# Kernel tuning notes

Measured on AMD Instinct MI355X. Metric: run time of the kernel, lower is better.

The kernel has to match this reference:

```python
import jax, jax.numpy as jnp
import numpy as np

MARGIN = 0.3
N, D, N_IDS = 8192, 128, 1024


def setup_inputs() -> dict:
    key = jax.random.key(0)
    k1, k2 = jax.random.split(key)
    inputs = jax.random.normal(k1, (N, D), dtype=jnp.float32)
    targets = jax.random.randint(k2, (N,), 0, N_IDS)
    return {"inputs": inputs, "targets": targets}


def reference(inputs, targets):
    # mask[i, j] = True iff sample j shares sample i's identity (includes j == i)
    mask = targets[:, None] == targets[None, :]               # [n, n] bool
    maskf = mask.astype(inputs.dtype)
    counts = maskf.sum(axis=1, keepdims=True)                 # [n, 1] (>= 1, self match)
    # center_i = mean of positives of sample i
    centers = (maskf @ inputs) / counts                       # [n, d]
    # squared distance from every center i to every sample j via gram expansion
    x2 = jnp.sum(inputs * inputs, axis=1)                     # [n]
    c2 = jnp.sum(centers * centers, axis=1)                   # [n]
    dist2 = c2[:, None] + x2[None, :] - 2.0 * (centers @ inputs.T)  # [n, n]
    # hard mining: farthest positive from center, closest negative to center
    dist_cp = jnp.where(mask, dist2, -jnp.inf).max(axis=1)    # [n]
    dist_cn = jnp.where(mask, jnp.inf, dist2).min(axis=1)     # [n]
    # MarginRankingLoss(y=1): mean(relu(-(dist_cn - dist_cp) + margin))
    loss = jnp.mean(jax.nn.relu(dist_cp - dist_cn + MARGIN))
    prec = jnp.mean((dist_cn > dist_cp).astype(jnp.float32))
    return loss, prec
```

## Files before the change

kernel.cpp:

```cpp
#include <hip/hip_runtime.h>
#include <math.h>

#define N_SAMPLES 8192
#define DIM 128
#define NCLS 1024
#define MARGIN_V 0.3f
#define DIST_GX (N_SAMPLES / 128)
#define DIST_GY (NCLS / 64)
#define NPART DIST_GX
#define MAXMEM 64
#define PIPE 16

using bf16x8 = __attribute__((ext_vector_type(8))) short;
using f32x16 = __attribute__((ext_vector_type(16))) float;
using short8 = __attribute__((ext_vector_type(8))) short;

__device__ __forceinline__ short bf16_rne(float x) {
  unsigned u = __float_as_uint(x);
  unsigned r = u + 0x7FFFu + ((u >> 16) & 1u);
  return (short)(r >> 16);
}

__device__ __forceinline__ size_t frag_idx(int row, int oct) {
  int tile = row >> 5, ks = oct >> 1, lane = ((oct & 1) << 5) | (row & 31);
  return (size_t)(tile * 8 + ks) * 64 + lane;
}

__global__ __launch_bounds__(256) void pack_kernel(
    const float* __restrict__ inputs, const int* __restrict__ targets,
    float* __restrict__ x2, float* __restrict__ c2, int* __restrict__ counts,
    short8* __restrict__ Apk, short8* __restrict__ Bpk, float* __restrict__ out) {
  int b = blockIdx.x;
  int tid = threadIdx.x;
  if (b == 0 && tid < 2) out[tid] = 0.f;
  if (b < N_SAMPLES / 16) {
    int row = b * 16 + (tid >> 4);
    int oct = tid & 15;
    const float4* p = (const float4*)(inputs + (size_t)row * DIM + oct * 8);
    float4 v0 = p[0], v1 = p[1];
    float v[8] = {v0.x, v0.y, v0.z, v0.w, v1.x, v1.y, v1.z, v1.w};
    float s = 0.f;
    #pragma unroll
    for (int i = 0; i < 8; i++) s += v[i] * v[i];
    #pragma unroll
    for (int m = 1; m < 16; m <<= 1) s += __shfl_xor(s, m);
    if (oct == 0) x2[row] = s;
    short8 hi;
    #pragma unroll
    for (int i = 0; i < 8; i++) hi[i] = bf16_rne(v[i]);
    Bpk[frag_idx(row, oct)] = hi;
  } else {
    __shared__ int mem[2][MAXMEM];
    __shared__ int mcnt[2];
    __shared__ float sctr[2][128];
    __shared__ float wsum[4];
    int c0 = (b - N_SAMPLES / 16) * 2;
    if (tid < 2) { mcnt[tid] = 0; mem[tid][0] = 0; }
    __syncthreads();
    int tg[N_SAMPLES / 256];
    #pragma unroll
    for (int i = 0; i < N_SAMPLES / 256; i++) tg[i] = targets[tid + 256 * i];
    #pragma unroll
    for (int i = 0; i < N_SAMPLES / 256; i++) {
      if (tg[i] == c0) {
        int p = atomicAdd(&mcnt[0], 1);
        if (p < MAXMEM) mem[0][p] = tid + 256 * i;
      } else if (tg[i] == c0 + 1) {
        int p = atomicAdd(&mcnt[1], 1);
        if (p < MAXMEM) mem[1][p] = tid + 256 * i;
      }
    }
    __syncthreads();
    int half = tid >> 7;
    int c = c0 + half;
    int d = tid & 127;
    int cnt = mcnt[half];
    int cl = (cnt < MAXMEM) ? cnt : MAXMEM;
    int n1 = (cl < PIPE) ? cl : PIPE;
    int idxs[PIPE];
    #pragma unroll
    for (int i = 0; i < PIPE; i++) idxs[i] = mem[half][(i < n1) ? i : 0];
    float vbuf[PIPE];
    #pragma unroll
    for (int i = 0; i < PIPE; i++) vbuf[i] = inputs[(size_t)idxs[i] * DIM + d];
    float acc = 0.f;
    #pragma unroll
    for (int i = 0; i < PIPE; i++) if (i < n1) acc += vbuf[i];
    for (int m = PIPE; m < cl; m++) acc += inputs[(size_t)mem[half][m] * DIM + d];
    float ctr = (cnt > 0) ? acc / (float)cnt : 0.f;
    sctr[half][d] = ctr;
    float vv = ctr * ctr;
    #pragma unroll
    for (int sh = 32; sh > 0; sh >>= 1) vv += __shfl_down(vv, sh);
    if ((tid & 63) == 0) wsum[tid >> 6] = vv;
    __syncthreads();
    if (d == 0) {
      c2[c] = wsum[half * 2] + wsum[half * 2 + 1];
      counts[c] = cnt;
    }
    if (d < 16) {
      int oct = d;
      short8 hi;
      #pragma unroll
      for (int i = 0; i < 8; i++) hi[i] = bf16_rne(sctr[half][oct * 8 + i]);
      Apk[frag_idx(c, oct)] = hi;
    }
  }
}

__global__ __launch_bounds__(256, 4) void dist_kernel(
    const short8* __restrict__ Apk, const short8* __restrict__ Bpk,
    const float* __restrict__ x2, const float* __restrict__ c2,
    const int* __restrict__ targets,
    float* __restrict__ dp_part, float* __restrict__ dn_part) {
  __shared__ float sc2[64];
  __shared__ float sx2[128];
  __shared__ int stgt[128];
  __shared__ float redp[2][2][32];
  __shared__ float redn[2][2][32];

  int tid = threadIdx.x;
  int jbase = blockIdx.x * 128;
  int cbase = blockIdx.y * 64;
  int wave = tid >> 6, lane = tid & 63;
  int wm = wave >> 1, wn = wave & 1;

  if (tid < 128) {
    sx2[tid] = x2[jbase + tid];
    stgt[tid] = targets[jbase + tid];
  }
  if (tid < 64) sc2[tid] = c2[cbase + tid];

  int mtg = (cbase >> 5) + wm;
  int ntg0 = (jbase >> 5) + wn * 2;

  f32x16 acc[2];
  acc[0] = (f32x16)(0.f);
  acc[1] = (f32x16)(0.f);

  #pragma unroll
  for (int ks = 0; ks < 8; ks++) {
    bf16x8 av = Apk[(size_t)(mtg * 8 + ks) * 64 + lane];
    bf16x8 b0 = Bpk[(size_t)((ntg0 + 0) * 8 + ks) * 64 + lane];
    bf16x8 b1 = Bpk[(size_t)((ntg0 + 1) * 8 + ks) * 64 + lane];
    acc[0] = __builtin_amdgcn_mfma_f32_32x32x16_bf16(av, b0, acc[0], 0, 0, 0);
    acc[1] = __builtin_amdgcn_mfma_f32_32x32x16_bf16(av, b1, acc[1], 0, 0, 0);
  }

  __syncthreads();

  int hf = lane >> 5;
  int col = lane & 31;
  #pragma unroll
  for (int r = 0; r < 16; r++) {
    int rowl = (r & 3) + 8 * (r >> 2) + 4 * hf;
    int c_loc = wm * 32 + rowl;
    int cg = cbase + c_loc;
    float c2v = sc2[c_loc];
    float pmax = -INFINITY, nmin = INFINITY;
    #pragma unroll
    for (int nt = 0; nt < 2; nt++) {
      int j_loc = wn * 64 + nt * 32 + col;
      float d2 = c2v + sx2[j_loc] - 2.f * acc[nt][r];
      if (stgt[j_loc] == cg) pmax = fmaxf(pmax, d2);
      else                   nmin = fminf(nmin, d2);
    }
    #pragma unroll
    for (int m = 1; m < 32; m <<= 1) {
      pmax = fmaxf(pmax, __shfl_xor(pmax, m));
      nmin = fminf(nmin, __shfl_xor(nmin, m));
    }
    if (col == 0) {
      redp[wn][wm][rowl] = pmax;
      redn[wn][wm][rowl] = nmin;
    }
  }
  __syncthreads();
  if (tid < 64) {
    int wmx = tid >> 5, idx = tid & 31;
    float dp = fmaxf(redp[0][wmx][idx], redp[1][wmx][idx]);
    float dn = fminf(redn[0][wmx][idx], redn[1][wmx][idx]);
    size_t slot = (size_t)blockIdx.x * NCLS + cbase + tid;
    dp_part[slot] = dp;
    dn_part[slot] = dn;
  }
}

__global__ __launch_bounds__(256) void finalize_kernel(
    const float* __restrict__ dp_part, const float* __restrict__ dn_part,
    const int* __restrict__ counts, float* __restrict__ out) {
  __shared__ float sdp[4][64];
  __shared__ float sdn[4][64];
  int g = blockIdx.x;
  int t = threadIdx.x;
  int cl = t & 63;
  int pg = t >> 6;
  int c = g * 64 + cl;
  float dp = -INFINITY, dn = INFINITY;
  #pragma unroll
  for (int p = pg * 16; p < pg * 16 + 16; p++) {
    dp = fmaxf(dp, dp_part[(size_t)p * NCLS + c]);
    dn = fminf(dn, dn_part[(size_t)p * NCLS + c]);
  }
  sdp[pg][cl] = dp;
  sdn[pg][cl] = dn;
  __syncthreads();
  if (t < 64) {
    dp = fmaxf(fmaxf(sdp[0][cl], sdp[1][cl]), fmaxf(sdp[2][cl], sdp[3][cl]));
    dn = fminf(fminf(sdn[0][cl], sdn[1][cl]), fminf(sdn[2][cl], sdn[3][cl]));
    int cnt = counts[c];
    float ls = 0.f, ps = 0.f;
    if (cnt > 0) {
      ls = (float)cnt * fmaxf(dp - dn + MARGIN_V, 0.f);
      ps = (float)cnt * ((dn > dp) ? 1.f : 0.f);
    }
    #pragma unroll
    for (int sh = 32; sh > 0; sh >>= 1) {
      ls += __shfl_down(ls, sh);
      ps += __shfl_down(ps, sh);
    }
    if (t == 0) {
      atomicAdd(&out[0], ls / (float)N_SAMPLES);
      atomicAdd(&out[1], ps / (float)N_SAMPLES);
    }
  }
}

extern "C" void kernel_launch(void* const* d_in, const int* in_sizes, int n_in,
                              void* d_out, int out_size, void* d_ws, size_t ws_size,
                              hipStream_t stream) {
  const float* inputs = (const float*)d_in[0];
  const int* targets = (const int*)d_in[1];
  float* out = (float*)d_out;

  char* w = (char*)d_ws;
  float* x2 = (float*)w;            w += (size_t)N_SAMPLES * 4;
  float* c2 = (float*)w;            w += (size_t)NCLS * 4;
  int* counts = (int*)w;            w += (size_t)NCLS * 4;
  float* dp_part = (float*)w;       w += (size_t)NPART * NCLS * 4;
  float* dn_part = (float*)w;       w += (size_t)NPART * NCLS * 4;
  short8* Apk = (short8*)w;         w += (size_t)NCLS * DIM * 2;
  short8* Bpk = (short8*)w;         w += (size_t)N_SAMPLES * DIM * 2;

  pack_kernel<<<N_SAMPLES / 16 + NCLS / 2, 256, 0, stream>>>(
      inputs, targets, x2, c2, counts, Apk, Bpk, out);
  dist_kernel<<<dim3(DIST_GX, DIST_GY), 256, 0, stream>>>(
      Apk, Bpk, x2, c2, targets, dp_part, dn_part);
  finalize_kernel<<<16, 256, 0, stream>>>(dp_part, dn_part, counts, out);
}
```

Measured before the change: 76.90 us.

## Fuse finalize into dist kernel via ordered-int atomics and last-block reduction

Replaces the per-block partial arrays and the separate finalize kernel with atomicMax/atomicMin on order-preserving unsigned encodings of the distances. A global counter identifies the last finishing block, which then computes the loss and precision directly. This removes one kernel launch and the partial-buffer traffic. In exchange it adds atomic contention on 1024 slots across 64 blocks per class group, plus a serialized tail reduction in a single block.

```diff
diff --git a/kernel.cpp b/kernel.cpp
--- a/kernel.cpp
+++ b/kernel.cpp
@@ -7,9 +7,9 @@
 #define MARGIN_V 0.3f
 #define DIST_GX (N_SAMPLES / 128)
 #define DIST_GY (NCLS / 64)
-#define NPART DIST_GX
 #define MAXMEM 64
 #define PIPE 16
+#define NBLK (DIST_GX * DIST_GY)
 
 using bf16x8 = __attribute__((ext_vector_type(8))) short;
 using f32x16 = __attribute__((ext_vector_type(16))) float;
@@ -21,6 +21,15 @@
   return (short)(r >> 16);
 }
 
+__device__ __forceinline__ unsigned f2ord(float f) {
+  unsigned u = __float_as_uint(f);
+  return (u & 0x80000000u) ? ~u : (u | 0x80000000u);
+}
+__device__ __forceinline__ float ord2f(unsigned k) {
+  unsigned v = (k & 0x80000000u) ? (k & 0x7FFFFFFFu) : ~k;
+  return __uint_as_float(v);
+}
+
 __device__ __forceinline__ size_t frag_idx(int row, int oct) {
   int tile = row >> 5, ks = oct >> 1, lane = ((oct & 1) << 5) | (row & 31);
   return (size_t)(tile * 8 + ks) * 64 + lane;
@@ -29,10 +38,12 @@
 __global__ __launch_bounds__(256) void pack_kernel(
     const float* __restrict__ inputs, const int* __restrict__ targets,
     float* __restrict__ x2, float* __restrict__ c2, int* __restrict__ counts,
-    short8* __restrict__ Apk, short8* __restrict__ Bpk, float* __restrict__ out) {
+    short8* __restrict__ Apk, short8* __restrict__ Bpk,
+    unsigned* __restrict__ dpk, unsigned* __restrict__ dnk,
+    int* __restrict__ ctr) {
   int b = blockIdx.x;
   int tid = threadIdx.x;
-  if (b == 0 && tid < 2) out[tid] = 0.f;
+  if (b == 0 && tid == 0) ctr[0] = 0;
   if (b < N_SAMPLES / 16) {
     int row = b * 16 + (tid >> 4);
     int oct = tid & 15;
@@ -87,9 +98,9 @@
     #pragma unroll
     for (int i = 0; i < PIPE; i++) if (i < n1) acc += vbuf[i];
     for (int m = PIPE; m < cl; m++) acc += inputs[(size_t)mem[half][m] * DIM + d];
-    float ctr = (cnt > 0) ? acc / (float)cnt : 0.f;
-    sctr[half][d] = ctr;
-    float vv = ctr * ctr;
+    float ctrv = (cnt > 0) ? acc / (float)cnt : 0.f;
+    sctr[half][d] = ctrv;
+    float vv = ctrv * ctrv;
     #pragma unroll
     for (int sh = 32; sh > 0; sh >>= 1) vv += __shfl_down(vv, sh);
     if ((tid & 63) == 0) wsum[tid >> 6] = vv;
@@ -97,6 +108,8 @@
     if (d == 0) {
       c2[c] = wsum[half * 2] + wsum[half * 2 + 1];
       counts[c] = cnt;
+      dpk[c] = 0u;
+      dnk[c] = 0xFFFFFFFFu;
     }
     if (d < 16) {
       int oct = d;
@@ -111,13 +124,16 @@
 __global__ __launch_bounds__(256, 4) void dist_kernel(
     const short8* __restrict__ Apk, const short8* __restrict__ Bpk,
     const float* __restrict__ x2, const float* __restrict__ c2,
-    const int* __restrict__ targets,
-    float* __restrict__ dp_part, float* __restrict__ dn_part) {
+    const int* __restrict__ targets, const int* __restrict__ counts,
+    unsigned* __restrict__ dpk, unsigned* __restrict__ dnk,
+    int* __restrict__ ctr, float* __restrict__ out) {
   __shared__ float sc2[64];
   __shared__ float sx2[128];
   __shared__ int stgt[128];
   __shared__ float redp[2][2][32];
   __shared__ float redn[2][2][32];
+  __shared__ int s_last;
+  __shared__ float fred[8];
 
   int tid = threadIdx.x;
   int jbase = blockIdx.x * 128;
@@ -180,49 +196,46 @@
     int wmx = tid >> 5, idx = tid & 31;
     float dp = fmaxf(redp[0][wmx][idx], redp[1][wmx][idx]);
     float dn = fminf(redn[0][wmx][idx], redn[1][wmx][idx]);
-    size_t slot = (size_t)blockIdx.x * NCLS + cbase + tid;
-    dp_part[slot] = dp;
-    dn_part[slot] = dn;
-  }
-}
-
-__global__ __launch_bounds__(256) void finalize_kernel(
-    const float* __restrict__ dp_part, const float* __restrict__ dn_part,
-    const int* __restrict__ counts, float* __restrict__ out) {
-  __shared__ float sdp[4][64];
-  __shared__ float sdn[4][64];
-  int g = blockIdx.x;
-  int t = threadIdx.x;
-  int cl = t & 63;
-  int pg = t >> 6;
-  int c = g * 64 + cl;
-  float dp = -INFINITY, dn = INFINITY;
-  #pragma unroll
-  for (int p = pg * 16; p < pg * 16 + 16; p++) {
-    dp = fmaxf(dp, dp_part[(size_t)p * NCLS + c]);
-    dn = fminf(dn, dn_part[(size_t)p * NCLS + c]);
-  }
-  sdp[pg][cl] = dp;
-  sdn[pg][cl] = dn;
-  __syncthreads();
-  if (t < 64) {
-    dp = fmaxf(fmaxf(sdp[0][cl], sdp[1][cl]), fmaxf(sdp[2][cl], sdp[3][cl]));
-    dn = fminf(fminf(sdn[0][cl], sdn[1][cl]), fminf(sdn[2][cl], sdn[3][cl]));
+    atomicMax(&dpk[cbase + tid], f2ord(dp));
+    atomicMin(&dnk[cbase + tid], f2ord(dn));
+  }
+
+  __syncthreads();
+  if (tid == 0) {
+    __threadfence();
+    int prev = __hip_atomic_fetch_add(ctr, 1, __ATOMIC_ACQ_REL,
+                                      __HIP_MEMORY_SCOPE_AGENT);
+    s_last = (prev == NBLK - 1) ? 1 : 0;
+  }
+  __syncthreads();
+  if (!s_last) return;
+  __threadfence();
+
+  float ls = 0.f, ps = 0.f;
+  #pragma unroll
+  for (int k = 0; k < 4; k++) {
+    int c = tid + 256 * k;
+    unsigned pk = __hip_atomic_load(&dpk[c], __ATOMIC_RELAXED,
+                                    __HIP_MEMORY_SCOPE_AGENT);
+    unsigned nk = __hip_atomic_load(&dnk[c], __ATOMIC_RELAXED,
+                                    __HIP_MEMORY_SCOPE_AGENT);
     int cnt = counts[c];
-    float ls = 0.f, ps = 0.f;
+    float dp = ord2f(pk), dn = ord2f(nk);
     if (cnt > 0) {
-      ls = (float)cnt * fmaxf(dp - dn + MARGIN_V, 0.f);
-      ps = (float)cnt * ((dn > dp) ? 1.f : 0.f);
-    }
-    #pragma unroll
-    for (int sh = 32; sh > 0; sh >>= 1) {
-      ls += __shfl_down(ls, sh);
-      ps += __shfl_down(ps, sh);
-    }
-    if (t == 0) {
-      atomicAdd(&out[0], ls / (float)N_SAMPLES);
-      atomicAdd(&out[1], ps / (float)N_SAMPLES);
-    }
+      ls += (float)cnt * fmaxf(dp - dn + MARGIN_V, 0.f);
+      ps += (float)cnt * ((dn > dp) ? 1.f : 0.f);
+    }
+  }
+  #pragma unroll
+  for (int sh = 32; sh > 0; sh >>= 1) {
+    ls += __shfl_down(ls, sh);
+    ps += __shfl_down(ps, sh);
+  }
+  if (lane == 0) { fred[wave] = ls; fred[4 + wave] = ps; }
+  __syncthreads();
+  if (tid == 0) {
+    out[0] = (fred[0] + fred[1] + fred[2] + fred[3]) / (float)N_SAMPLES;
+    out[1] = (fred[4] + fred[5] + fred[6] + fred[7]) / (float)N_SAMPLES;
   }
 }
 
@@ -234,17 +247,17 @@
   float* out = (float*)d_out;
 
   char* w = (char*)d_ws;
+  int* ctr = (int*)w;               w += 16;
   float* x2 = (float*)w;            w += (size_t)N_SAMPLES * 4;
   float* c2 = (float*)w;            w += (size_t)NCLS * 4;
   int* counts = (int*)w;            w += (size_t)NCLS * 4;
-  float* dp_part = (float*)w;       w += (size_t)NPART * NCLS * 4;
-  float* dn_part = (float*)w;       w += (size_t)NPART * NCLS * 4;
+  unsigned* dpk = (unsigned*)w;     w += (size_t)NCLS * 4;
+  unsigned* dnk = (unsigned*)w;     w += (size_t)NCLS * 4;
   short8* Apk = (short8*)w;         w += (size_t)NCLS * DIM * 2;
   short8* Bpk = (short8*)w;         w += (size_t)N_SAMPLES * DIM * 2;
 
   pack_kernel<<<N_SAMPLES / 16 + NCLS / 2, 256, 0, stream>>>(
-      inputs, targets, x2, c2, counts, Apk, Bpk, out);
+      inputs, targets, x2, c2, counts, Apk, Bpk, dpk, dnk, ctr);
   dist_kernel<<<dim3(DIST_GX, DIST_GY), 256, 0, stream>>>(
-      Apk, Bpk, x2, c2, targets, dp_part, dn_part);
-  finalize_kernel<<<16, 256, 0, stream>>>(dp_part, dn_part, counts, out);
-}
+      Apk, Bpk, x2, c2, targets, counts, dpk, dnk, ctr, out);
+}
```

Measured after the change: 103.1 us. 1.34x slower.

## Swap MFMA operands so row reductions stay in-lane and prefetch all fragments

Applied to the files above, without the earlier changes.

The MFMA operands are swapped so each lane's accumulator column maps to one center, which turns the per-row max/min reduction into an in-register loop followed by a single cross-half shuffle, replacing 16 rows of five-step butterfly shuffles. All A and B fragments are loaded into registers before the MFMA loop to expose more memory-level parallelism. The occupancy hint drops from 4 to 3 blocks per SM to make room for the extra registers. The distance kernel's epilogue is its main shuffle-heavy cost, so this targets that work at the price of lower occupancy.

```diff
diff --git a/kernel.cpp b/kernel.cpp
--- a/kernel.cpp
+++ b/kernel.cpp
@@ -87,9 +87,9 @@
     #pragma unroll
     for (int i = 0; i < PIPE; i++) if (i < n1) acc += vbuf[i];
     for (int m = PIPE; m < cl; m++) acc += inputs[(size_t)mem[half][m] * DIM + d];
-    float ctr = (cnt > 0) ? acc / (float)cnt : 0.f;
-    sctr[half][d] = ctr;
-    float vv = ctr * ctr;
+    float ctrv = (cnt > 0) ? acc / (float)cnt : 0.f;
+    sctr[half][d] = ctrv;
+    float vv = ctrv * ctrv;
     #pragma unroll
     for (int sh = 32; sh > 0; sh >>= 1) vv += __shfl_down(vv, sh);
     if ((tid & 63) == 0) wsum[tid >> 6] = vv;
@@ -108,7 +108,7 @@
   }
 }
 
-__global__ __launch_bounds__(256, 4) void dist_kernel(
+__global__ __launch_bounds__(256, 3) void dist_kernel(
     const short8* __restrict__ Apk, const short8* __restrict__ Bpk,
     const float* __restrict__ x2, const float* __restrict__ c2,
     const int* __restrict__ targets,
@@ -134,46 +134,50 @@
   int mtg = (cbase >> 5) + wm;
   int ntg0 = (jbase >> 5) + wn * 2;
 
+  const short8* abase  = &Apk[(size_t)(mtg * 8) * 64 + lane];
+  const short8* b0base = &Bpk[(size_t)((ntg0 + 0) * 8) * 64 + lane];
+  const short8* b1base = &Bpk[(size_t)((ntg0 + 1) * 8) * 64 + lane];
+  bf16x8 av[8], b0[8], b1[8];
+  #pragma unroll
+  for (int ks = 0; ks < 8; ks++) {
+    av[ks] = abase[(size_t)ks * 64];
+    b0[ks] = b0base[(size_t)ks * 64];
+    b1[ks] = b1base[(size_t)ks * 64];
+  }
+
   f32x16 acc[2];
   acc[0] = (f32x16)(0.f);
   acc[1] = (f32x16)(0.f);
 
   #pragma unroll
   for (int ks = 0; ks < 8; ks++) {
-    bf16x8 av = Apk[(size_t)(mtg * 8 + ks) * 64 + lane];
-    bf16x8 b0 = Bpk[(size_t)((ntg0 + 0) * 8 + ks) * 64 + lane];
-    bf16x8 b1 = Bpk[(size_t)((ntg0 + 1) * 8 + ks) * 64 + lane];
-    acc[0] = __builtin_amdgcn_mfma_f32_32x32x16_bf16(av, b0, acc[0], 0, 0, 0);
-    acc[1] = __builtin_amdgcn_mfma_f32_32x32x16_bf16(av, b1, acc[1], 0, 0, 0);
+    acc[0] = __builtin_amdgcn_mfma_f32_32x32x16_bf16(b0[ks], av[ks], acc[0], 0, 0, 0);
+    acc[1] = __builtin_amdgcn_mfma_f32_32x32x16_bf16(b1[ks], av[ks], acc[1], 0, 0, 0);
   }
 
   __syncthreads();
 
+  int col = lane & 31;
   int hf = lane >> 5;
-  int col = lane & 31;
-  #pragma unroll
-  for (int r = 0; r < 16; r++) {
-    int rowl = (r & 3) + 8 * (r >> 2) + 4 * hf;
-    int c_loc = wm * 32 + rowl;
-    int cg = cbase + c_loc;
-    float c2v = sc2[c_loc];
-    float pmax = -INFINITY, nmin = INFINITY;
-    #pragma unroll
-    for (int nt = 0; nt < 2; nt++) {
-      int j_loc = wn * 64 + nt * 32 + col;
+  int c_loc = wm * 32 + col;
+  int cg = cbase + c_loc;
+  float c2v = sc2[c_loc];
+  float pmax = -INFINITY, nmin = INFINITY;
+  #pragma unroll
+  for (int nt = 0; nt < 2; nt++) {
+    #pragma unroll
+    for (int r = 0; r < 16; r++) {
+      int j_loc = wn * 64 + nt * 32 + (r & 3) + 8 * (r >> 2) + 4 * hf;
       float d2 = c2v + sx2[j_loc] - 2.f * acc[nt][r];
       if (stgt[j_loc] == cg) pmax = fmaxf(pmax, d2);
       else                   nmin = fminf(nmin, d2);
     }
-    #pragma unroll
-    for (int m = 1; m < 32; m <<= 1) {
-      pmax = fmaxf(pmax, __shfl_xor(pmax, m));
-      nmin = fminf(nmin, __shfl_xor(nmin, m));
-    }
-    if (col == 0) {
-      redp[wn][wm][rowl] = pmax;
-      redn[wn][wm][rowl] = nmin;
-    }
+  }
+  pmax = fmaxf(pmax, __shfl_xor(pmax, 32));
+  nmin = fminf(nmin, __shfl_xor(nmin, 32));
+  if (lane < 32) {
+    redp[wn][wm][col] = pmax;
+    redn[wn][wm][col] = nmin;
   }
   __syncthreads();
   if (tid < 64) {
```

New measurement: 69.88 us. 1.1x faster.
